# Performance work log

Hardware: AMD Instinct MI355X
Metric: run time of the kernel (lower is better)

The kernel has to match this reference:

```python
import jax, jax.numpy as jnp
import numpy as np

N, D_IN, D, K = 8192, 1024, 256, 30
SCALE = D ** (-0.5)


def setup_inputs() -> dict:
    key = jax.random.key(0)
    ks = jax.random.split(key, 10)
    p = lambda k, sh: (jax.random.normal(k, sh, dtype=jnp.float32) * 0.02)
    return {
        'x_path': jax.random.normal(ks[0], (N, D_IN), dtype=jnp.float32),
        'W_fc1': p(ks[1], (D_IN, D)), 'b_fc1': jnp.zeros((D,), jnp.float32),
        'W_fc2': p(ks[2], (D, D)),   'b_fc2': jnp.zeros((D,), jnp.float32),
        'W_head': p(ks[3], (D, D)),  'b_head': jnp.zeros((D,), jnp.float32),
        'W_tail': p(ks[4], (D, D)),  'b_tail': jnp.zeros((D,), jnp.float32),
        'W_lin1': p(ks[5], (D, D)),  'b_lin1': jnp.zeros((D,), jnp.float32),
        'W_lin2': p(ks[6], (D, D)),  'b_lin2': jnp.zeros((D,), jnp.float32),
        'W_att1': p(ks[7], (D, D // 2)), 'b_att1': jnp.zeros((D // 2,), jnp.float32),
        'W_att2': p(ks[8], (D // 2, 1)), 'b_att2': jnp.zeros((1,), jnp.float32),
    }


def reference(x_path, W_fc1, b_fc1, W_fc2, b_fc2, W_head, b_head, W_tail, b_tail,
              W_lin1, b_lin1, W_lin2, b_lin2, W_att1, b_att1, W_att2, b_att2):
    # pathology_fc (eval mode, dropout = identity): 1024 -> 256 -> 256
    h = jax.nn.relu(x_path @ W_fc1 + b_fc1)
    h = jax.nn.relu(h @ W_fc2 + b_fc2)                      # [N, D]

    e_h = h @ W_head + b_head                               # [N, D]
    e_t = h @ W_tail + b_tail                               # [N, D]

    # pairwise scores + topk neighbor selection
    attn_logit = (e_h * SCALE) @ e_t.T                      # [N, N]
    topk_w, topk_i = jax.lax.top_k(attn_logit, K)           # [N, K]
    topk_prob = jax.nn.softmax(topk_w, axis=-1)             # [N, K]

    Nb_h = e_t[topk_i]                                      # gather neighbors [N, K, D]

    # gated message construction
    eh_r = topk_prob[..., None] * Nb_h + (1.0 - topk_prob)[..., None] * e_h[:, None, :]
    gate = jnp.tanh(e_h[:, None, :] + eh_r)                 # [N, K, D]

    # torch.einsum('ijkl,ijkm->ijk', Nb_h, gate): l and m summed independently
    ka_weight = Nb_h.sum(-1) * gate.sum(-1)                 # [N, K]
    ka_prob = jax.nn.softmax(ka_weight, axis=-1)            # [N, K]
    e_Nh = jnp.einsum('nk,nkd->nd', ka_prob, Nb_h)          # [N, D]

    sum_emb = jax.nn.relu((e_h + e_Nh) @ W_lin1 + b_lin1)
    bi_emb = jax.nn.relu((e_h * e_Nh) @ W_lin2 + b_lin2)
    e = sum_emb + bi_emb                                    # [N, D]

    # GlobalAttention readout
    att = jax.nn.leaky_relu(e @ W_att1 + b_att1, 0.01) @ W_att2 + b_att2   # [N, 1]
    a = jax.nn.softmax(att, axis=0)                         # softmax over nodes
    e_g = (a * e).sum(0)                                    # [D]
    return e, e_g
```

## Files before the change

kernel.cpp:

```cpp
#include <hip/hip_runtime.h>
#include <math.h>

#define NN   8192
#define DIN  1024
#define DD   256
#define TOPK 30
#define KP   40
#define CAP  88
#define NINF -3e38f

typedef short s8v  __attribute__((ext_vector_type(8)));
typedef float f16v __attribute__((ext_vector_type(16)));

__device__ __forceinline__ float wred_sum(float v) {
  v += __shfl_down(v, 32); v += __shfl_down(v, 16); v += __shfl_down(v, 8);
  v += __shfl_down(v, 4);  v += __shfl_down(v, 2);  v += __shfl_down(v, 1);
  return v;
}
__device__ __forceinline__ float wred_max(float v) {
  v = fmaxf(v, __shfl_down(v, 32)); v = fmaxf(v, __shfl_down(v, 16));
  v = fmaxf(v, __shfl_down(v, 8));  v = fmaxf(v, __shfl_down(v, 4));
  v = fmaxf(v, __shfl_down(v, 2));  v = fmaxf(v, __shfl_down(v, 1));
  return v;
}
__device__ __forceinline__ float tanh_fast(float x) {
  return 1.f - 2.f / (__expf(2.f * x) + 1.f);
}
__device__ __forceinline__ unsigned short f2bf(float x) {
  union { float f; unsigned int u; } v; v.f = x;
  unsigned int r = v.u + 0x7FFF + ((v.u >> 16) & 1);
  return (unsigned short)(r >> 16);
}
__device__ __forceinline__ bool pair_gt(float v, int i, float pv, int pi) {
  return (v > pv) || (v == pv && i < pi);
}
__device__ __forceinline__ unsigned key_pack(float f, int col) {
  unsigned b = __float_as_uint(f);
  unsigned u = ((int)b < 0) ? ~b : (b | 0x80000000u);
  return (u & 0xFFFFE000u) | (unsigned)col;
}

template<int ACT, int AOP, int ACCUM>
__global__ __launch_bounds__(128, 4)
void gemm_k(const float* __restrict__ A, const float* __restrict__ A2,
            const float* __restrict__ B, const float* __restrict__ bias,
            float* __restrict__ C, int K, int NB)
{
  __shared__ float sA[32 * 36];
  __shared__ float sB[32 * 68];
  const int t  = threadIdx.x;
  const int rb = blockIdx.x * 32;
  const int cb = blockIdx.y * 64;
  const int tr = t >> 4;
  const int tc = t & 15;

  float acc[4][4];
#pragma unroll
  for (int u = 0; u < 4; ++u)
#pragma unroll
    for (int j = 0; j < 4; ++j) acc[u][j] = 0.f;

  const int sr  = t >> 2;
  const int sk2 = (t & 3) * 4;

  for (int kt = 0; kt < K; kt += 32) {
    __syncthreads();
    {
      const float* Ap = A + (size_t)(rb + sr) * K + kt;
      float4 va = *(const float4*)(Ap + sk2);
      float4 vb = *(const float4*)(Ap + sk2 + 16);
      if (AOP) {
        const float* A2p = A2 + (size_t)(rb + sr) * K + kt;
        const float4 wa = *(const float4*)(A2p + sk2);
        const float4 wb = *(const float4*)(A2p + sk2 + 16);
        if (AOP == 1) {
          va.x += wa.x; va.y += wa.y; va.z += wa.z; va.w += wa.w;
          vb.x += wb.x; vb.y += wb.y; vb.z += wb.z; vb.w += wb.w;
        } else {
          va.x *= wa.x; va.y *= wa.y; va.z *= wa.z; va.w *= wa.w;
          vb.x *= wb.x; vb.y *= wb.y; vb.z *= wb.z; vb.w *= wb.w;
        }
      }
      sA[(sk2 + 0) * 36 + sr] = va.x; sA[(sk2 + 1) * 36 + sr] = va.y;
      sA[(sk2 + 2) * 36 + sr] = va.z; sA[(sk2 + 3) * 36 + sr] = va.w;
      sA[(sk2 + 16) * 36 + sr] = vb.x; sA[(sk2 + 17) * 36 + sr] = vb.y;
      sA[(sk2 + 18) * 36 + sr] = vb.z; sA[(sk2 + 19) * 36 + sr] = vb.w;
    }
    {
#pragma unroll
      for (int i = 0; i < 4; ++i) {
        const int f4 = t + 128 * i;
        const int k  = f4 >> 4;
        const int c4 = (f4 & 15) << 2;
        *(float4*)&sB[k * 68 + c4] = *(const float4*)&B[(size_t)(kt + k) * NB + cb + c4];
      }
    }
    __syncthreads();
#pragma unroll 8
    for (int k = 0; k < 32; ++k) {
      const float4 bv = *(const float4*)&sB[k * 68 + 4 * tc];
      const float4 av = *(const float4*)&sA[k * 36 + 4 * tr];
      const float a[4] = {av.x, av.y, av.z, av.w};
      const float b[4] = {bv.x, bv.y, bv.z, bv.w};
#pragma unroll
      for (int u = 0; u < 4; ++u)
#pragma unroll
        for (int j = 0; j < 4; ++j) acc[u][j] = fmaf(a[u], b[j], acc[u][j]);
    }
  }

  const float4 bz = *(const float4*)&bias[cb + 4 * tc];
  const float bb[4] = {bz.x, bz.y, bz.z, bz.w};
#pragma unroll
  for (int u = 0; u < 4; ++u) {
    const int row = rb + 4 * tr + u;
    float o[4];
#pragma unroll
    for (int j = 0; j < 4; ++j) {
      o[j] = acc[u][j] + bb[j];
      if (ACT) o[j] = fmaxf(o[j], 0.f);
    }
    float* Cp = &C[(size_t)row * NB + cb + 4 * tc];
    if (ACCUM) {
      const float4 old = *(const float4*)Cp;
      o[0] += old.x; o[1] += old.y; o[2] += old.z; o[3] += old.w;
    }
    float4 ov; ov.x = o[0]; ov.y = o[1]; ov.z = o[2]; ov.w = o[3];
    *(float4*)Cp = ov;
  }
}

__global__ __launch_bounds__(256)
void pack_frag_k(const float* __restrict__ src, unsigned short* __restrict__ dst)
{
  const int c = blockIdx.x * 256 + threadIdx.x;
  const int l = c & 63;
  const int W = (c >> 6) & 15;
  const int T = c >> 10;
  const int col = T * 32 + (l & 31);
  const int k0  = W * 16 + ((l >> 5) << 3);
  const float4 a = *(const float4*)&src[(size_t)col * DD + k0];
  const float4 b = *(const float4*)&src[(size_t)col * DD + k0 + 4];
  uint4 o;
  o.x = (unsigned)f2bf(a.x) | ((unsigned)f2bf(a.y) << 16);
  o.y = (unsigned)f2bf(a.z) | ((unsigned)f2bf(a.w) << 16);
  o.z = (unsigned)f2bf(b.x) | ((unsigned)f2bf(b.y) << 16);
  o.w = (unsigned)f2bf(b.z) | ((unsigned)f2bf(b.w) << 16);
  *(uint4*)&dst[(size_t)c * 8] = o;
}

__global__ __launch_bounds__(256)
void rowsum_k(const float* __restrict__ et, float* __restrict__ rs)
{
  const int t = threadIdx.x, lane = t & 63, w = t >> 6;
  const int n = blockIdx.x * 4 + w;
  const float4 v = *(const float4*)&et[(size_t)n * DD + lane * 4];
  float s = v.x + v.y + v.z + v.w;
  s = wred_sum(s);
  if (lane == 0) rs[n] = s;
}

__global__ __launch_bounds__(512, 4)
void score_cand_k(const unsigned short* __restrict__ ehF,
                  const unsigned short* __restrict__ etF,
                  unsigned* __restrict__ gCand)
{
  __shared__ unsigned sBuf[32 * CAP];
  __shared__ unsigned sK[32][KP];
  __shared__ unsigned sThrK[32];
  __shared__ int      sCnt[32];

  const int t = threadIdx.x, lane = t & 63, w = t >> 6;
  const int g  = blockIdx.x;
  const int sy = blockIdx.y;
  const int tile0 = sy * 128;
  const s8v* eh8 = (const s8v*)ehF;
  const s8v* et8 = (const s8v*)etF;

  s8v af[16];
#pragma unroll
  for (int W = 0; W < 16; ++W)
    af[W] = eh8[((size_t)g * 16 + W) * 64 + lane];

  for (int idx = t; idx < 32 * KP; idx += 512) ((unsigned*)sK)[idx] = 0u;
  if (t < 32) { sThrK[t] = 0u; sCnt[t] = 0; }
  __syncthreads();

  const int rq = 4 * (lane >> 5);
  const int colLane = lane & 31;
  const int leader = (lane >> 5) << 5;
  const unsigned lm = (1u << (lane & 31)) - 1;

  int tb = 0;
  for (int rnd = 0; rnd < 7; ++rnd) {
    const int ntile = (rnd == 0) ? 2 : (2 << (rnd - 1));
    for (int p = w; p < ntile; p += 8) {
      const int T = tile0 + tb + p;
      const s8v* bp = et8 + (size_t)T * 1024 + lane;
      f16v c;
#pragma unroll
      for (int i = 0; i < 16; ++i) c[i] = 0.f;
      {
        s8v b[8];
#pragma unroll
        for (int q = 0; q < 8; ++q) b[q] = bp[q * 64];
#pragma unroll
        for (int q = 0; q < 8; ++q)
          c = __builtin_amdgcn_mfma_f32_32x32x16_bf16(af[q], b[q], c, 0, 0, 0);
#pragma unroll
        for (int q = 0; q < 8; ++q) b[q] = bp[(8 + q) * 64];
#pragma unroll
        for (int q = 0; q < 8; ++q)
          c = __builtin_amdgcn_mfma_f32_32x32x16_bf16(af[8 + q], b[q], c, 0, 0, 0);
      }
      const int col = T * 32 + colLane;
#pragma unroll
      for (int r = 0; r < 16; ++r) {
        const int row = (r & 3) + 8 * (r >> 2) + rq;
        const unsigned key = key_pack(c[r], col);
        const bool pass = key > sThrK[row];
        const unsigned long long mask = __ballot(pass);
        if (mask) {
          const unsigned hm = (unsigned)(mask >> leader);
          int base = 0;
          if ((lane & 31) == 0) base = atomicAdd(&sCnt[row], __popc(hm));
          base = __shfl(base, leader);
          if (pass) {
            const int ix = base + __popc(hm & lm);
            if (ix < CAP) sBuf[row * CAP + ix] = key;
          }
        }
      }
    }
    __syncthreads();

#pragma unroll 1
    for (int rp = 0; rp < 2; ++rp) {
      const int ra = 4 * w + 2 * rp;
      const int rc = ra + 1;
      const int cA = min(sCnt[ra], CAP);
      const int cB = min(sCnt[rc], CAP);
      unsigned a0 = (lane < KP) ? sK[ra][lane]
                                : ((lane - KP) < cA ? sBuf[ra * CAP + (lane - KP)] : 0u);
      unsigned a1 = ((24 + lane) < cA) ? sBuf[ra * CAP + 24 + lane] : 0u;
      unsigned b0 = (lane < KP) ? sK[rc][lane]
                                : ((lane - KP) < cB ? sBuf[rc * CAP + (lane - KP)] : 0u);
      unsigned b1 = ((24 + lane) < cB) ? sBuf[rc * CAP + 24 + lane] : 0u;
#pragma unroll
      for (int k = 2; k <= 128; k <<= 1) {
#pragma unroll
        for (int j = k >> 1; j >= 1; j >>= 1) {
          if (j == 64) {
            unsigned mx = max(a0, a1), mn = min(a0, a1); a0 = mx; a1 = mn;
            mx = max(b0, b1); mn = min(b0, b1); b0 = mx; b1 = mn;
          } else {
            const unsigned pa0 = (unsigned)__shfl_xor((int)a0, j);
            const unsigned pa1 = (unsigned)__shfl_xor((int)a1, j);
            const unsigned pb0 = (unsigned)__shfl_xor((int)b0, j);
            const unsigned pb1 = (unsigned)__shfl_xor((int)b1, j);
            const bool km0 = (((lane & k) == 0)        == ((lane & j) == 0));
            const bool km1 = ((((64 + lane) & k) == 0) == ((lane & j) == 0));
            a0 = km0 ? max(a0, pa0) : min(a0, pa0);
            a1 = km1 ? max(a1, pa1) : min(a1, pa1);
            b0 = km0 ? max(b0, pb0) : min(b0, pb0);
            b1 = km1 ? max(b1, pb1) : min(b1, pb1);
          }
        }
      }
      if (rnd < 6) {
        if (lane < KP) { sK[ra][lane] = a0; sK[rc][lane] = b0; }
        if (lane == KP - 1) { sThrK[ra] = a0; sThrK[rc] = b0; }
        if (lane == 0) { sCnt[ra] = 0; sCnt[rc] = 0; }
      } else {
        if (lane < KP) {
          gCand[(((size_t)g * 2 + sy) * 32 + ra) * KP + lane] = a0;
          gCand[(((size_t)g * 2 + sy) * 32 + rc) * KP + lane] = b0;
        }
      }
    }
    __syncthreads();
    tb += ntile;
  }
}

__global__ __launch_bounds__(512, 2)
void cand_merge_k(const unsigned* __restrict__ gCand,
                  const float* __restrict__ e_h, const float* __restrict__ e_t,
                  float* __restrict__ topv_g, int* __restrict__ topi_g)
{
  __shared__ float    sEh[16 * 256];
  __shared__ unsigned sK40[16][KP];
  __shared__ float    sRes[16][KP];
  const int t = threadIdx.x, lane = t & 63, w = t >> 6;
  const int g = blockIdx.x, rb = g * 32;
  const int r0 = blockIdx.y * 16;

  for (int i = t; i < 1024; i += 512)
    ((float4*)sEh)[i] = ((const float4*)(e_h + (size_t)(rb + r0) * 256))[i];

#pragma unroll 1
  for (int rp = 0; rp < 2; ++rp) {
    const int lr = 2 * w + rp;
    const int r  = r0 + lr;
    unsigned v0, v1;
    {
      const int m = lane;
      const int s = m / 40, q = m - s * 40;
      v0 = gCand[(((size_t)g * 2 + s) * 32 + r) * KP + q];
    }
    {
      const int m = 64 + lane;
      if (m < 80) {
        const int q = m - 40;
        v1 = gCand[(((size_t)g * 2 + 1) * 32 + r) * KP + q];
      } else v1 = 0u;
    }
#pragma unroll
    for (int k = 2; k <= 128; k <<= 1) {
#pragma unroll
      for (int j = k >> 1; j >= 1; j >>= 1) {
        if (j == 64) {
          const unsigned mx = max(v0, v1), mn = min(v0, v1);
          v0 = mx; v1 = mn;
        } else {
          const unsigned p0 = (unsigned)__shfl_xor((int)v0, j);
          const unsigned p1 = (unsigned)__shfl_xor((int)v1, j);
          const bool km0 = (((lane & k) == 0)        == ((lane & j) == 0));
          const bool km1 = ((((64 + lane) & k) == 0) == ((lane & j) == 0));
          v0 = km0 ? max(v0, p0) : min(v0, p0);
          v1 = km1 ? max(v1, p1) : min(v1, p1);
        }
      }
    }
    if (lane < KP) sK40[lr][lane] = v0;
  }
  __syncthreads();

  for (int i = t; i < 16 * KP; i += 512) {
    const int lr = i / KP, q = i - lr * KP;
    const int c = (int)(sK40[lr][q] & 0x1FFFu);
    const float* et = &e_t[(size_t)c * 256];
    const float* eh = &sEh[lr * 256];
    float acc = 0.f;
#pragma unroll 8
    for (int d = 0; d < 64; ++d) {
      const float4 a = *(const float4*)&eh[d * 4];
      const float4 b = *(const float4*)&et[d * 4];
      acc = fmaf(a.x, b.x, acc); acc = fmaf(a.y, b.y, acc);
      acc = fmaf(a.z, b.z, acc); acc = fmaf(a.w, b.w, acc);
    }
    sRes[lr][q] = acc * 0.0625f;
  }
  __syncthreads();

#pragma unroll 1
  for (int rp = 0; rp < 2; ++rp) {
    const int lr = 2 * w + rp;
    float v; int c;
    if (lane < KP) { v = sRes[lr][lane]; c = (int)(sK40[lr][lane] & 0x1FFFu); }
    else           { v = NINF;           c = 0x40000000 + lane; }
#pragma unroll
    for (int k = 2; k <= 64; k <<= 1) {
#pragma unroll
      for (int j = k >> 1; j >= 1; j >>= 1) {
        const float pv = __shfl_xor(v, j);
        const int   pc = __shfl_xor(c, j);
        const bool km = (((lane & k) == 0) == ((lane & j) == 0));
        const bool gt = pair_gt(v, c, pv, pc);
        const bool keep = (km == gt);
        v = keep ? v : pv; c = keep ? c : pc;
      }
    }
    if (lane < TOPK) {
      topv_g[(size_t)(rb + r0 + lr) * TOPK + lane] = v;
      topi_g[(size_t)(rb + r0 + lr) * TOPK + lane] = c;
    }
  }
}

__global__ __launch_bounds__(256)
void message_k(const float* __restrict__ e_h, const float* __restrict__ e_t,
               const float* __restrict__ rs, const float* __restrict__ tv_g,
               const int* __restrict__ ti_g, float* __restrict__ e_Nh)
{
  __shared__ float sP[TOPK];
  __shared__ int   sI[TOPK];
  __shared__ float sW[TOPK];
  __shared__ float wpart[TOPK][4];
  const int n = blockIdx.x;
  const int t = threadIdx.x, lane = t & 63, w = t >> 6;

  if (w == 0) {
    const float v = (lane < TOPK) ? tv_g[(size_t)n * TOPK + lane] : NINF;
    float m = wred_max(v); m = __shfl(m, 0);
    const float p = (lane < TOPK) ? __expf(v - m) : 0.f;
    float s = wred_sum(p); s = __shfl(s, 0);
    if (lane < TOPK) { sP[lane] = p / s; sI[lane] = ti_g[(size_t)n * TOPK + lane]; }
  }
  __syncthreads();

  const float eh = e_h[(size_t)n * DD + t];
  float nbv[TOPK];
  float gg[TOPK];
#pragma unroll
  for (int k = 0; k < TOPK; ++k) {
    const int   j = sI[k];
    const float p = sP[k];
    const float nb = e_t[(size_t)j * DD + t];
    nbv[k] = nb;
    gg[k] = tanh_fast((2.f - p) * eh + p * nb);
  }
#pragma unroll
  for (int off = 32; off >= 1; off >>= 1)
#pragma unroll
    for (int k = 0; k < TOPK; ++k)
      gg[k] += __shfl_down(gg[k], off);
  if (lane == 0)
#pragma unroll
    for (int k = 0; k < TOPK; ++k) wpart[k][w] = gg[k];
  __syncthreads();

  if (w == 0) {
    float kw = NINF;
    if (lane < TOPK) {
      const float gs = wpart[lane][0] + wpart[lane][1] + wpart[lane][2] + wpart[lane][3];
      kw = rs[sI[lane]] * gs;
    }
    float m = wred_max(kw); m = __shfl(m, 0);
    const float p = (lane < TOPK) ? __expf(kw - m) : 0.f;
    float s = wred_sum(p); s = __shfl(s, 0);
    if (lane < TOPK) sW[lane] = p / s;
  }
  __syncthreads();

  float o = 0.f;
#pragma unroll
  for (int k = 0; k < TOPK; ++k) o = fmaf(sW[k], nbv[k], o);
  e_Nh[(size_t)n * DD + t] = o;
}

__global__ __launch_bounds__(256)
void att_k(const float* __restrict__ e, const float* __restrict__ W1,
           const float* __restrict__ b1, const float* __restrict__ W2,
           const float* __restrict__ b2, float* __restrict__ att)
{
  const int t = threadIdx.x;
  const int q = t >> 7;
  const int m = t & 127;
  const int lane = t & 63, w = t >> 6;
  const int n0 = blockIdx.x * 8 + q * 4;
  float acc[4] = {0.f, 0.f, 0.f, 0.f};
  for (int d = 0; d < DD; ++d) {
    const float wv = W1[d * 128 + m];
#pragma unroll
    for (int rr = 0; rr < 4; ++rr)
      acc[rr] = fmaf(e[(size_t)(n0 + rr) * DD + d], wv, acc[rr]);
  }
  const float b1m = b1[m], w2m = W2[m];
  __shared__ float part[4][4];
#pragma unroll
  for (int rr = 0; rr < 4; ++rr) {
    float v = acc[rr] + b1m;
    v = (v > 0.f) ? v : 0.01f * v;
    v *= w2m;
    v = wred_sum(v);
    if (lane == 0) part[w][rr] = v;
  }
  __syncthreads();
  if (t < 8) {
    const int qq = t >> 2, rr = t & 3;
    att[blockIdx.x * 8 + qq * 4 + rr] = part[qq * 2][rr] + part[qq * 2 + 1][rr] + b2[0];
  }
}

__global__ __launch_bounds__(1024)
void smax_prep_k(const float* __restrict__ att, float* __restrict__ stats,
                 float* __restrict__ eg)
{
  __shared__ float red[16];
  __shared__ float mg;
  const int t = threadIdx.x, lane = t & 63, w = t >> 6;
  float m = NINF;
#pragma unroll
  for (int i = 0; i < 8; ++i) m = fmaxf(m, att[t + 1024 * i]);
  m = wred_max(m);
  if (lane == 0) red[w] = m;
  __syncthreads();
  if (t == 0) {
    float mm = red[0];
    for (int i = 1; i < 16; ++i) mm = fmaxf(mm, red[i]);
    mg = mm;
  }
  __syncthreads();
  const float mm = mg;
  float s = 0.f;
#pragma unroll
  for (int i = 0; i < 8; ++i) s += __expf(att[t + 1024 * i] - mm);
  s = wred_sum(s);
  __syncthreads();
  if (lane == 0) red[w] = s;
  __syncthreads();
  if (t == 0) {
    float ss = 0.f;
    for (int i = 0; i < 16; ++i) ss += red[i];
    stats[0] = mm; stats[1] = ss;
  }
  if (t < DD) eg[t] = 0.f;
}

__global__ __launch_bounds__(256)
void eg_k(const float* __restrict__ att, const float* __restrict__ stats,
          const float* __restrict__ e, float* __restrict__ eg)
{
  const int t = threadIdx.x;
  const float m = stats[0], inv = 1.f / stats[1];
  float acc = 0.f;
  const int n0 = blockIdx.x * 128;
  for (int r = 0; r < 128; ++r) {
    const int n = n0 + r;
    acc = fmaf(__expf(att[n] - m), e[(size_t)n * DD + t], acc);
  }
  atomicAdd(&eg[t], acc * inv);
}

extern "C" void kernel_launch(void* const* d_in, const int* in_sizes, int n_in,
                              void* d_out, int out_size, void* d_ws, size_t ws_size,
                              hipStream_t stream)
{
  const float* x      = (const float*)d_in[0];
  const float* W_fc1  = (const float*)d_in[1];
  const float* b_fc1  = (const float*)d_in[2];
  const float* W_fc2  = (const float*)d_in[3];
  const float* b_fc2  = (const float*)d_in[4];
  const float* W_head = (const float*)d_in[5];
  const float* b_head = (const float*)d_in[6];
  const float* W_tail = (const float*)d_in[7];
  const float* b_tail = (const float*)d_in[8];
  const float* W_lin1 = (const float*)d_in[9];
  const float* b_lin1 = (const float*)d_in[10];
  const float* W_lin2 = (const float*)d_in[11];
  const float* b_lin2 = (const float*)d_in[12];
  const float* W_att1 = (const float*)d_in[13];
  const float* b_att1 = (const float*)d_in[14];
  const float* W_att2 = (const float*)d_in[15];
  const float* b_att2 = (const float*)d_in[16];

  float* out_e  = (float*)d_out;
  float* out_eg = out_e + (size_t)NN * DD;

  float* ws = (float*)d_ws;
  const size_t F = (size_t)NN * DD;
  float* e_h   = ws;
  float* e_t   = ws + F;
  float* e_Nh  = ws + 2 * F;
  float* bufA  = ws + 3 * F;
  float* bufB  = ws + 4 * F;
  float* rs    = ws + 5 * F;
  float* att   = rs + NN;
  float* stats = att + NN;
  float* topv  = stats + 16;
  int*   topi  = (int*)(topv + (size_t)NN * TOPK);

  unsigned short* ehF = (unsigned short*)bufA;
  unsigned short* etF = ehF + F;
  unsigned* gCand = (unsigned*)bufB;

  const dim3 blk(256);
  const dim3 gblk(128);
  const dim3 gemmGrid(NN / 32, DD / 64);

  gemm_k<1,0,0><<<gemmGrid, gblk, 0, stream>>>(x,    nullptr, W_fc1, b_fc1, bufA, DIN, DD);
  gemm_k<1,0,0><<<gemmGrid, gblk, 0, stream>>>(bufA, nullptr, W_fc2, b_fc2, bufB, DD,  DD);
  gemm_k<0,0,0><<<gemmGrid, gblk, 0, stream>>>(bufB, nullptr, W_head, b_head, e_h, DD, DD);
  gemm_k<0,0,0><<<gemmGrid, gblk, 0, stream>>>(bufB, nullptr, W_tail, b_tail, e_t, DD, DD);

  pack_frag_k<<<dim3(NN * DD / 8 / 256), blk, 0, stream>>>(e_h, ehF);
  pack_frag_k<<<dim3(NN * DD / 8 / 256), blk, 0, stream>>>(e_t, etF);
  rowsum_k<<<dim3(NN / 4), blk, 0, stream>>>(e_t, rs);

  score_cand_k<<<dim3(NN / 32, 2), dim3(512), 0, stream>>>(ehF, etF, gCand);
  cand_merge_k<<<dim3(NN / 32, 2), dim3(512), 0, stream>>>(gCand, e_h, e_t, topv, topi);

  message_k<<<dim3(NN), blk, 0, stream>>>(e_h, e_t, rs, topv, topi, e_Nh);

  gemm_k<1,1,0><<<gemmGrid, gblk, 0, stream>>>(e_h, e_Nh, W_lin1, b_lin1, out_e, DD, DD);
  gemm_k<1,2,1><<<gemmGrid, gblk, 0, stream>>>(e_h, e_Nh, W_lin2, b_lin2, out_e, DD, DD);

  att_k<<<dim3(NN / 8), blk, 0, stream>>>(out_e, W_att1, b_att1, W_att2, b_att2, att);
  smax_prep_k<<<dim3(1), dim3(1024), 0, stream>>>(att, stats, out_eg);
  eg_k<<<dim3(64), blk, 0, stream>>>(att, stats, out_e, out_eg);
}
```

Baseline: 664.9 us.

## Fuse head/tail and lin1/lin2 GEMMs, merge pack launches, simplify candidate insertion

Merges the head and tail projections into one dual-output GEMM that loads each A tile once, and fuses the lin1/lin2 GEMMs into one kernel that forms sum and product inputs in shared memory and writes the combined ReLU output directly. This removes the second read of e_h/e_Nh and the read-modify-write of out_e. The two pack launches become one 2D-grid launch. In the candidate scan, the ballot/popc warp-aggregated append is replaced with a per-lane shared atomicAdd, which simplifies the code but may add atomic contention. The fused GEMMs also use more registers and LDS, which could lower occupancy.

```diff
diff --git a/kernel.cpp b/kernel.cpp
--- a/kernel.cpp
+++ b/kernel.cpp
@@ -40,9 +40,9 @@
   return (u & 0xFFFFE000u) | (unsigned)col;
 }
 
-template<int ACT, int AOP, int ACCUM>
+template<int ACT>
 __global__ __launch_bounds__(128, 4)
-void gemm_k(const float* __restrict__ A, const float* __restrict__ A2,
+void gemm_k(const float* __restrict__ A,
             const float* __restrict__ B, const float* __restrict__ bias,
             float* __restrict__ C, int K, int NB)
 {
@@ -69,18 +69,6 @@
       const float* Ap = A + (size_t)(rb + sr) * K + kt;
       float4 va = *(const float4*)(Ap + sk2);
       float4 vb = *(const float4*)(Ap + sk2 + 16);
-      if (AOP) {
-        const float* A2p = A2 + (size_t)(rb + sr) * K + kt;
-        const float4 wa = *(const float4*)(A2p + sk2);
-        const float4 wb = *(const float4*)(A2p + sk2 + 16);
-        if (AOP == 1) {
-          va.x += wa.x; va.y += wa.y; va.z += wa.z; va.w += wa.w;
-          vb.x += wb.x; vb.y += wb.y; vb.z += wb.z; vb.w += wb.w;
-        } else {
-          va.x *= wa.x; va.y *= wa.y; va.z *= wa.z; va.w *= wa.w;
-          vb.x *= wb.x; vb.y *= wb.y; vb.z *= wb.z; vb.w *= wb.w;
-        }
-      }
       sA[(sk2 + 0) * 36 + sr] = va.x; sA[(sk2 + 1) * 36 + sr] = va.y;
       sA[(sk2 + 2) * 36 + sr] = va.z; sA[(sk2 + 3) * 36 + sr] = va.w;
       sA[(sk2 + 16) * 36 + sr] = vb.x; sA[(sk2 + 17) * 36 + sr] = vb.y;
@@ -120,19 +108,189 @@
       o[j] = acc[u][j] + bb[j];
       if (ACT) o[j] = fmaxf(o[j], 0.f);
     }
-    float* Cp = &C[(size_t)row * NB + cb + 4 * tc];
-    if (ACCUM) {
-      const float4 old = *(const float4*)Cp;
-      o[0] += old.x; o[1] += old.y; o[2] += old.z; o[3] += old.w;
-    }
     float4 ov; ov.x = o[0]; ov.y = o[1]; ov.z = o[2]; ov.w = o[3];
-    *(float4*)Cp = ov;
+    *(float4*)&C[(size_t)row * NB + cb + 4 * tc] = ov;
+  }
+}
+
+__global__ __launch_bounds__(128, 4)
+void gemm2_k(const float* __restrict__ A,
+             const float* __restrict__ B1, const float* __restrict__ bias1,
+             float* __restrict__ C1,
+             const float* __restrict__ B2, const float* __restrict__ bias2,
+             float* __restrict__ C2, int K, int NB)
+{
+  __shared__ float sA[32 * 36];
+  __shared__ float sB1[32 * 68];
+  __shared__ float sB2[32 * 68];
+  const int t  = threadIdx.x;
+  const int rb = blockIdx.x * 32;
+  const int cb = blockIdx.y * 64;
+  const int tr = t >> 4;
+  const int tc = t & 15;
+
+  float acc1[4][4], acc2[4][4];
+#pragma unroll
+  for (int u = 0; u < 4; ++u)
+#pragma unroll
+    for (int j = 0; j < 4; ++j) { acc1[u][j] = 0.f; acc2[u][j] = 0.f; }
+
+  const int sr  = t >> 2;
+  const int sk2 = (t & 3) * 4;
+
+  for (int kt = 0; kt < K; kt += 32) {
+    __syncthreads();
+    {
+      const float* Ap = A + (size_t)(rb + sr) * K + kt;
+      float4 va = *(const float4*)(Ap + sk2);
+      float4 vb = *(const float4*)(Ap + sk2 + 16);
+      sA[(sk2 + 0) * 36 + sr] = va.x; sA[(sk2 + 1) * 36 + sr] = va.y;
+      sA[(sk2 + 2) * 36 + sr] = va.z; sA[(sk2 + 3) * 36 + sr] = va.w;
+      sA[(sk2 + 16) * 36 + sr] = vb.x; sA[(sk2 + 17) * 36 + sr] = vb.y;
+      sA[(sk2 + 18) * 36 + sr] = vb.z; sA[(sk2 + 19) * 36 + sr] = vb.w;
+    }
+    {
+#pragma unroll
+      for (int i = 0; i < 4; ++i) {
+        const int f4 = t + 128 * i;
+        const int k  = f4 >> 4;
+        const int c4 = (f4 & 15) << 2;
+        *(float4*)&sB1[k * 68 + c4] = *(const float4*)&B1[(size_t)(kt + k) * NB + cb + c4];
+        *(float4*)&sB2[k * 68 + c4] = *(const float4*)&B2[(size_t)(kt + k) * NB + cb + c4];
+      }
+    }
+    __syncthreads();
+#pragma unroll 4
+    for (int k = 0; k < 32; ++k) {
+      const float4 b1 = *(const float4*)&sB1[k * 68 + 4 * tc];
+      const float4 b2 = *(const float4*)&sB2[k * 68 + 4 * tc];
+      const float4 av = *(const float4*)&sA[k * 36 + 4 * tr];
+      const float a[4] = {av.x, av.y, av.z, av.w};
+      const float v1[4] = {b1.x, b1.y, b1.z, b1.w};
+      const float v2[4] = {b2.x, b2.y, b2.z, b2.w};
+#pragma unroll
+      for (int u = 0; u < 4; ++u)
+#pragma unroll
+        for (int j = 0; j < 4; ++j) {
+          acc1[u][j] = fmaf(a[u], v1[j], acc1[u][j]);
+          acc2[u][j] = fmaf(a[u], v2[j], acc2[u][j]);
+        }
+    }
+  }
+
+  const float4 z1 = *(const float4*)&bias1[cb + 4 * tc];
+  const float4 z2 = *(const float4*)&bias2[cb + 4 * tc];
+  const float c1b[4] = {z1.x, z1.y, z1.z, z1.w};
+  const float c2b[4] = {z2.x, z2.y, z2.z, z2.w};
+#pragma unroll
+  for (int u = 0; u < 4; ++u) {
+    const int row = rb + 4 * tr + u;
+    float4 o1, o2;
+    o1.x = acc1[u][0] + c1b[0]; o1.y = acc1[u][1] + c1b[1];
+    o1.z = acc1[u][2] + c1b[2]; o1.w = acc1[u][3] + c1b[3];
+    o2.x = acc2[u][0] + c2b[0]; o2.y = acc2[u][1] + c2b[1];
+    o2.z = acc2[u][2] + c2b[2]; o2.w = acc2[u][3] + c2b[3];
+    *(float4*)&C1[(size_t)row * NB + cb + 4 * tc] = o1;
+    *(float4*)&C2[(size_t)row * NB + cb + 4 * tc] = o2;
+  }
+}
+
+__global__ __launch_bounds__(128, 4)
+void gemm_lin_k(const float* __restrict__ Eh, const float* __restrict__ En,
+                const float* __restrict__ B1, const float* __restrict__ bias1,
+                const float* __restrict__ B2, const float* __restrict__ bias2,
+                float* __restrict__ C, int K, int NB)
+{
+  __shared__ float sA1[32 * 36];
+  __shared__ float sA2[32 * 36];
+  __shared__ float sB1[32 * 68];
+  __shared__ float sB2[32 * 68];
+  const int t  = threadIdx.x;
+  const int rb = blockIdx.x * 32;
+  const int cb = blockIdx.y * 64;
+  const int tr = t >> 4;
+  const int tc = t & 15;
+
+  float acc1[4][4], acc2[4][4];
+#pragma unroll
+  for (int u = 0; u < 4; ++u)
+#pragma unroll
+    for (int j = 0; j < 4; ++j) { acc1[u][j] = 0.f; acc2[u][j] = 0.f; }
+
+  const int sr  = t >> 2;
+  const int sk2 = (t & 3) * 4;
+
+  for (int kt = 0; kt < K; kt += 32) {
+    __syncthreads();
+    {
+      const float* Hp = Eh + (size_t)(rb + sr) * K + kt;
+      const float* Np = En + (size_t)(rb + sr) * K + kt;
+      const float4 ha = *(const float4*)(Hp + sk2);
+      const float4 hb = *(const float4*)(Hp + sk2 + 16);
+      const float4 na = *(const float4*)(Np + sk2);
+      const float4 nb = *(const float4*)(Np + sk2 + 16);
+      sA1[(sk2 + 0) * 36 + sr] = ha.x + na.x; sA2[(sk2 + 0) * 36 + sr] = ha.x * na.x;
+      sA1[(sk2 + 1) * 36 + sr] = ha.y + na.y; sA2[(sk2 + 1) * 36 + sr] = ha.y * na.y;
+      sA1[(sk2 + 2) * 36 + sr] = ha.z + na.z; sA2[(sk2 + 2) * 36 + sr] = ha.z * na.z;
+      sA1[(sk2 + 3) * 36 + sr] = ha.w + na.w; sA2[(sk2 + 3) * 36 + sr] = ha.w * na.w;
+      sA1[(sk2 + 16) * 36 + sr] = hb.x + nb.x; sA2[(sk2 + 16) * 36 + sr] = hb.x * nb.x;
+      sA1[(sk2 + 17) * 36 + sr] = hb.y + nb.y; sA2[(sk2 + 17) * 36 + sr] = hb.y * nb.y;
+      sA1[(sk2 + 18) * 36 + sr] = hb.z + nb.z; sA2[(sk2 + 18) * 36 + sr] = hb.z * nb.z;
+      sA1[(sk2 + 19) * 36 + sr] = hb.w + nb.w; sA2[(sk2 + 19) * 36 + sr] = hb.w * nb.w;
+    }
+    {
+#pragma unroll
+      for (int i = 0; i < 4; ++i) {
+        const int f4 = t + 128 * i;
+        const int k  = f4 >> 4;
+        const int c4 = (f4 & 15) << 2;
+        *(float4*)&sB1[k * 68 + c4] = *(const float4*)&B1[(size_t)(kt + k) * NB + cb + c4];
+        *(float4*)&sB2[k * 68 + c4] = *(const float4*)&B2[(size_t)(kt + k) * NB + cb + c4];
+      }
+    }
+    __syncthreads();
+#pragma unroll 4
+    for (int k = 0; k < 32; ++k) {
+      const float4 b1 = *(const float4*)&sB1[k * 68 + 4 * tc];
+      const float4 b2 = *(const float4*)&sB2[k * 68 + 4 * tc];
+      const float4 a1 = *(const float4*)&sA1[k * 36 + 4 * tr];
+      const float4 a2 = *(const float4*)&sA2[k * 36 + 4 * tr];
+      const float x1[4] = {a1.x, a1.y, a1.z, a1.w};
+      const float x2[4] = {a2.x, a2.y, a2.z, a2.w};
+      const float v1[4] = {b1.x, b1.y, b1.z, b1.w};
+      const float v2[4] = {b2.x, b2.y, b2.z, b2.w};
+#pragma unroll
+      for (int u = 0; u < 4; ++u)
+#pragma unroll
+        for (int j = 0; j < 4; ++j) {
+          acc1[u][j] = fmaf(x1[u], v1[j], acc1[u][j]);
+          acc2[u][j] = fmaf(x2[u], v2[j], acc2[u][j]);
+        }
+    }
+  }
+
+  const float4 z1 = *(const float4*)&bias1[cb + 4 * tc];
+  const float4 z2 = *(const float4*)&bias2[cb + 4 * tc];
+  const float c1b[4] = {z1.x, z1.y, z1.z, z1.w};
+  const float c2b[4] = {z2.x, z2.y, z2.z, z2.w};
+#pragma unroll
+  for (int u = 0; u < 4; ++u) {
+    const int row = rb + 4 * tr + u;
+    float4 ov;
+    ov.x = fmaxf(acc1[u][0] + c1b[0], 0.f) + fmaxf(acc2[u][0] + c2b[0], 0.f);
+    ov.y = fmaxf(acc1[u][1] + c1b[1], 0.f) + fmaxf(acc2[u][1] + c2b[1], 0.f);
+    ov.z = fmaxf(acc1[u][2] + c1b[2], 0.f) + fmaxf(acc2[u][2] + c2b[2], 0.f);
+    ov.w = fmaxf(acc1[u][3] + c1b[3], 0.f) + fmaxf(acc2[u][3] + c2b[3], 0.f);
+    *(float4*)&C[(size_t)row * NB + cb + 4 * tc] = ov;
   }
 }
 
 __global__ __launch_bounds__(256)
-void pack_frag_k(const float* __restrict__ src, unsigned short* __restrict__ dst)
-{
+void pack_frag_k(const float* __restrict__ srcA, unsigned short* __restrict__ dstA,
+                 const float* __restrict__ srcB, unsigned short* __restrict__ dstB)
+{
+  const float* src = blockIdx.y ? srcB : srcA;
+  unsigned short* dst = blockIdx.y ? dstB : dstA;
   const int c = blockIdx.x * 256 + threadIdx.x;
   const int l = c & 63;
   const int W = (c >> 6) & 15;
@@ -188,8 +346,6 @@
 
   const int rq = 4 * (lane >> 5);
   const int colLane = lane & 31;
-  const int leader = (lane >> 5) << 5;
-  const unsigned lm = (1u << (lane & 31)) - 1;
 
   int tb = 0;
   for (int rnd = 0; rnd < 7; ++rnd) {
@@ -218,17 +374,9 @@
       for (int r = 0; r < 16; ++r) {
         const int row = (r & 3) + 8 * (r >> 2) + rq;
         const unsigned key = key_pack(c[r], col);
-        const bool pass = key > sThrK[row];
-        const unsigned long long mask = __ballot(pass);
-        if (mask) {
-          const unsigned hm = (unsigned)(mask >> leader);
-          int base = 0;
-          if ((lane & 31) == 0) base = atomicAdd(&sCnt[row], __popc(hm));
-          base = __shfl(base, leader);
-          if (pass) {
-            const int ix = base + __popc(hm & lm);
-            if (ix < CAP) sBuf[row * CAP + ix] = key;
-          }
+        if (key > sThrK[row]) {
+          const int ix = atomicAdd(&sCnt[row], 1);
+          if (ix < CAP) sBuf[row * CAP + ix] = key;
         }
       }
     }
@@ -569,13 +717,12 @@
   const dim3 gblk(128);
   const dim3 gemmGrid(NN / 32, DD / 64);
 
-  gemm_k<1,0,0><<<gemmGrid, gblk, 0, stream>>>(x,    nullptr, W_fc1, b_fc1, bufA, DIN, DD);
-  gemm_k<1,0,0><<<gemmGrid, gblk, 0, stream>>>(bufA, nullptr, W_fc2, b_fc2, bufB, DD,  DD);
-  gemm_k<0,0,0><<<gemmGrid, gblk, 0, stream>>>(bufB, nullptr, W_head, b_head, e_h, DD, DD);
-  gemm_k<0,0,0><<<gemmGrid, gblk, 0, stream>>>(bufB, nullptr, W_tail, b_tail, e_t, DD, DD);
-
-  pack_frag_k<<<dim3(NN * DD / 8 / 256), blk, 0, stream>>>(e_h, ehF);
-  pack_frag_k<<<dim3(NN * DD / 8 / 256), blk, 0, stream>>>(e_t, etF);
+  gemm_k<1><<<gemmGrid, gblk, 0, stream>>>(x,    W_fc1, b_fc1, bufA, DIN, DD);
+  gemm_k<1><<<gemmGrid, gblk, 0, stream>>>(bufA, W_fc2, b_fc2, bufB, DD,  DD);
+  gemm2_k<<<gemmGrid, gblk, 0, stream>>>(bufB, W_head, b_head, e_h,
+                                         W_tail, b_tail, e_t, DD, DD);
+
+  pack_frag_k<<<dim3(NN * DD / 8 / 256, 2), blk, 0, stream>>>(e_h, ehF, e_t, etF);
   rowsum_k<<<dim3(NN / 4), blk, 0, stream>>>(e_t, rs);
 
   score_cand_k<<<dim3(NN / 32, 2), dim3(512), 0, stream>>>(ehF, etF, gCand);
@@ -583,8 +730,8 @@
 
   message_k<<<dim3(NN), blk, 0, stream>>>(e_h, e_t, rs, topv, topi, e_Nh);
 
-  gemm_k<1,1,0><<<gemmGrid, gblk, 0, stream>>>(e_h, e_Nh, W_lin1, b_lin1, out_e, DD, DD);
-  gemm_k<1,2,1><<<gemmGrid, gblk, 0, stream>>>(e_h, e_Nh, W_lin2, b_lin2, out_e, DD, DD);
+  gemm_lin_k<<<gemmGrid, gblk, 0, stream>>>(e_h, e_Nh, W_lin1, b_lin1,
+                                            W_lin2, b_lin2, out_e, DD, DD);
 
   att_k<<<dim3(NN / 8), blk, 0, stream>>>(out_e, W_att1, b_att1, W_att2, b_att2, att);
   smax_prep_k<<<dim3(1), dim3(1024), 0, stream>>>(att, stats, out_eg);
```

Measured after the change: 626.0 us. 5.9% less time.
